# Kernel tuning notes

Measured on AMD Instinct MI355X. Metric: run time of the kernel, lower is better.

Reference implementation:

```python
import jax, jax.numpy as jnp
import numpy as np
from jax import lax

B, N, T, H, V, C = 256, 196, 26, 512, 12000, 1000


def setup_inputs() -> dict:
    key = jax.random.key(0)
    ks = jax.random.split(key, 24)
    g = lambda i, shape, s=0.02: jax.random.normal(ks[i], shape, jnp.float32) * s
    z = lambda *shape: jnp.zeros(shape, jnp.float32)
    return {
        "image": jax.random.normal(ks[0], (B, N, H), jnp.float32),
        "question": jax.random.randint(ks[1], (B, T), 0, V, jnp.int32),
        "embed_table": g(2, (V, H), 1.0),
        "W_img": g(3, (H, H)), "b_img": z(H),
        "W_uni": g(4, (1, H, H)), "b_uni": z(H),
        "W_bi": g(5, (2, H, H)), "b_bi": z(H),
        "W_tri": g(6, (3, H, H)), "b_tri": z(H),
        "lstm_k": g(7, (H, 4 * H)), "lstm_rk": g(8, (H, 4 * H)), "lstm_b": z(4 * H),
        "W_corr": g(9, (H, H)), "b_corr": z(H),
        "W_qe": g(10, (H, H)), "b_qe": z(H),
        "W_ie": g(11, (H, H)), "b_ie": z(H),
        "w_qa": g(12, (H, 1)), "b_qa": z(1),
        "w_ia": g(13, (H, 1)), "b_ia": z(1),
        "W_w": g(14, (H, H)), "b_w": z(H),
        "W_p": g(15, (2 * H, H)), "b_p": z(H),
        "W_s": g(16, (2 * H, H)), "b_s": z(H),
        "W_fc1": g(17, (H, 2 * H)), "b_fc1": z(2 * H),
        "W_fc": g(18, (2 * H, C)), "b_fc": z(C),
    }


def _conv1d(x, w, b, dil):
    # x: [B,T,H], w: [k, in, out] (WIO). TF 'same' padding == XLA SAME.
    y = lax.conv_general_dilated(x, w, window_strides=(1,), padding='SAME',
                                 rhs_dilation=(dil,),
                                 dimension_numbers=('NWC', 'WIO', 'NWC'))
    return y + b


def _lstm(x, k, rk, b):
    # Keras LSTM, gate order i,f,c,o; inference (dropout off).
    xp = jnp.einsum('bth,hg->btg', x, k) + b  # [B,T,4H]
    h0 = jnp.zeros((x.shape[0], rk.shape[0]), x.dtype)

    def step(carry, xt):
        h, c = carry
        zg = xt + h @ rk
        i, f, g, o = jnp.split(zg, 4, axis=-1)
        i, f, o = jax.nn.sigmoid(i), jax.nn.sigmoid(f), jax.nn.sigmoid(o)
        c = f * c + i * jnp.tanh(g)
        h = o * jnp.tanh(c)
        return (h, c), h

    _, hs = lax.scan(step, (h0, h0), jnp.swapaxes(xp, 0, 1))
    return jnp.swapaxes(hs, 0, 1)  # [B,T,H]


def _co_attention(img_feat, ques_feat, W_corr, b_corr, W_qe, b_qe, W_ie, b_ie,
                  w_qa, b_qa, w_ia, b_ia):
    img_corr = img_feat @ W_corr + b_corr                       # [B,N,H]
    wm = jnp.tanh(jnp.einsum('btd,bnd->btn', ques_feat, img_corr))  # affinity
    ques_embed = ques_feat @ W_qe + b_qe                        # [B,T,H]
    img_embed = img_feat @ W_ie + b_ie                          # [B,N,H]
    ques_sum = jnp.tanh(jnp.einsum('btn,bnd->btd', wm, img_embed) + ques_embed)
    ques_att = jax.nn.softmax((ques_sum @ w_qa + b_qa)[..., 0], axis=-1)  # [B,T]
    img_sum = jnp.tanh(jnp.einsum('btn,btd->bnd', wm, ques_embed) + img_embed)
    img_att = jax.nn.softmax((img_sum @ w_ia + b_ia)[..., 0], axis=-1)    # [B,N]
    q_feat = jnp.einsum('bt,btd->bd', ques_att, ques_feat)
    v_feat = jnp.einsum('bn,bnd->bd', img_att, img_feat)
    return v_feat, q_feat


def reference(image, question, embed_table, W_img, b_img, W_uni, b_uni, W_bi, b_bi,
              W_tri, b_tri, lstm_k, lstm_rk, lstm_b, W_corr, b_corr, W_qe, b_qe,
              W_ie, b_ie, w_qa, b_qa, w_ia, b_ia, W_w, b_w, W_p, b_p, W_s, b_s,
              W_fc1, b_fc1, W_fc, b_fc):
    img = jnp.tanh(image @ W_img + b_img)                       # [B,N,H]
    words = embed_table[question]                               # [B,T,H]
    uni = jnp.tanh(_conv1d(words, W_uni, b_uni, 1))
    bi = jnp.tanh(_conv1d(words, W_bi, b_bi, 2))
    tri = jnp.tanh(_conv1d(words, W_tri, b_tri, 2))
    phrase = jnp.tanh(jnp.maximum(jnp.maximum(uni, bi), tri))   # maxpool over 3 n-grams
    sentence = _lstm(phrase, lstm_k, lstm_rk, lstm_b)
    ca = lambda v, q: _co_attention(v, q, W_corr, b_corr, W_qe, b_qe, W_ie, b_ie,
                                    w_qa, b_qa, w_ia, b_ia)
    v_word, q_word = ca(img, words)
    v_phr, q_phr = ca(img, phrase)
    v_sent, q_sent = ca(img, sentence)
    h_w = jnp.tanh((q_word + v_word) @ W_w + b_w)
    h_p = jnp.tanh(jnp.concatenate([q_phr + v_phr, h_w], axis=1) @ W_p + b_p)
    h_s = jnp.tanh(jnp.concatenate([q_sent + v_sent, h_p], axis=1) @ W_s + b_s)
    fc1 = jax.nn.relu(h_s @ W_fc1 + b_fc1)
    return jax.nn.softmax(fc1 @ W_fc + b_fc, axis=-1)           # [B,C]
```

## Files before the change

### kernel.cpp

```cpp
#include <hip/hip_runtime.h>
#include <hip/hip_bf16.h>
#include <math.h>

#define Bq   256
#define Nimg 196
#define Tseq 26
#define Hd   512
#define H4   2048
#define Ccls 1000
#define KP   1536

typedef int   int4v  __attribute__((ext_vector_type(4)));
typedef float f32x4  __attribute__((ext_vector_type(4)));

#define SWZ8(x) ((x) ^ (((x) >> 3) & 7))

__device__ __forceinline__ float fast_tanh(float x) {
    float e = __expf(2.0f * x);
    return 1.0f - 2.0f * __builtin_amdgcn_rcpf(e + 1.0f);
}
__device__ __forceinline__ float fast_sigmoid(float x) {
    return __builtin_amdgcn_rcpf(1.0f + __expf(-x));
}

__device__ __forceinline__ short f2bf(float x) {
    union { float f; unsigned u; } a; a.f = x;
    unsigned r = a.u + 0x7FFF + ((a.u >> 16) & 1);
    return (short)(r >> 16);
}
__device__ __forceinline__ float bf2f(short b) {
    union { float f; unsigned u; } a; a.u = ((unsigned)(unsigned short)b) << 16;
    return a.f;
}

__global__ void embed_kernel(const int* __restrict__ q, const float* __restrict__ table,
                             short* __restrict__ words2) {
    int row = blockIdx.x;
    int tok = q[row];
    int c4 = threadIdx.x * 4;
    float4 v = *reinterpret_cast<const float4*>(table + (size_t)tok * Hd + c4);
    short h0 = f2bf(v.x), h1 = f2bf(v.y), h2 = f2bf(v.z), h3 = f2bf(v.w);
    short l0 = f2bf(v.x - bf2f(h0)), l1 = f2bf(v.y - bf2f(h1));
    short l2 = f2bf(v.z - bf2f(h2)), l3 = f2bf(v.w - bf2f(h3));
    *reinterpret_cast<short4*>(words2 + (size_t)row * 1024 + c4) = make_short4(h0, h1, h2, h3);
    *reinterpret_cast<short4*>(words2 + (size_t)row * 1024 + 512 + c4) = make_short4(l0, l1, l2, l3);
}

__global__ void split_kernel(const float* __restrict__ X, short* __restrict__ X2) {
    int i4 = blockIdx.x * 256 + threadIdx.x;
    int m = i4 >> 7, c4 = (i4 & 127) * 4;
    float4 v = *reinterpret_cast<const float4*>(X + ((size_t)m << 9) + c4);
    short h0 = f2bf(v.x), h1 = f2bf(v.y), h2 = f2bf(v.z), h3 = f2bf(v.w);
    short l0 = f2bf(v.x - bf2f(h0)), l1 = f2bf(v.y - bf2f(h1));
    short l2 = f2bf(v.z - bf2f(h2)), l3 = f2bf(v.w - bf2f(h3));
    *reinterpret_cast<short4*>(X2 + (size_t)m * 1024 + c4) = make_short4(h0, h1, h2, h3);
    *reinterpret_cast<short4*>(X2 + (size_t)m * 1024 + 512 + c4) = make_short4(l0, l1, l2, l3);
}

__global__ __launch_bounds__(256) void wsplit_all_kernel(
    const float* __restrict__ W_img, const float* __restrict__ W_corr,
    const float* __restrict__ W_ie, const float* __restrict__ W_qe,
    const float* __restrict__ W_uni, const float* __restrict__ W_bi,
    const float* __restrict__ W_tri, const float* __restrict__ lstm_k,
    short* __restrict__ WimgT2, short* __restrict__ WcorrT2,
    short* __restrict__ WieT2, short* __restrict__ WqeT2,
    short* __restrict__ WconvT2, short* __restrict__ lkT2) {
    const int z = blockIdx.z;
    const float* W; short* WT2; int Nw, n0;
    const size_t HK = (size_t)Hd * KP;
    if (z < 10) {
        Nw = Hd; n0 = blockIdx.x * 64;
        switch (z) {
            case 0: W = W_img;  WT2 = WimgT2;  break;
            case 1: W = W_corr; WT2 = WcorrT2; break;
            case 2: W = W_ie;   WT2 = WieT2;   break;
            case 3: W = W_qe;   WT2 = WqeT2;   break;
            case 4: W = W_uni;                     WT2 = WconvT2 + 0 * HK; break;
            case 5: W = W_bi;                      WT2 = WconvT2 + 1 * HK; break;
            case 6: W = W_bi + (size_t)Hd * Hd;    WT2 = WconvT2 + 2 * HK; break;
            case 7: W = W_tri;                     WT2 = WconvT2 + 3 * HK; break;
            case 8: W = W_tri + (size_t)Hd * Hd;   WT2 = WconvT2 + 4 * HK; break;
            default:W = W_tri + 2 * (size_t)Hd * Hd; WT2 = WconvT2 + 5 * HK; break;
        }
    } else {
        Nw = H4; W = lstm_k; WT2 = lkT2;
        n0 = ((z - 10) * 8 + blockIdx.x) * 64;
    }
    __shared__ float tile[64][65];
    const int k0 = blockIdx.y * 64;
    const int tid = threadIdx.x;
    #pragma unroll
    for (int p = 0; p < 16; ++p) {
        int r = p * 4 + (tid >> 6);
        int c = tid & 63;
        tile[r][c] = W[(size_t)(k0 + r) * Nw + n0 + c];
    }
    __syncthreads();
    const int n = tid >> 2;
    const int ksub = (tid & 3) * 16;
    size_t base = (size_t)(n0 + n) * KP + k0 + ksub;
    #pragma unroll
    for (int k = 0; k < 16; ++k) {
        float x = tile[ksub + k][n];
        short h = f2bf(x);
        short l = f2bf(x - bf2f(h));
        WT2[base + k] = h;
        WT2[base + 512 + k] = h;
        WT2[base + 1024 + k] = l;
    }
}

__device__ __forceinline__ void mfma16(f32x4& acc, int4v a, int4v b) {
    asm volatile("v_mfma_f32_16x16x32_bf16 %0, %1, %2, %0" : "+v"(acc) : "v"(a), "v"(b));
}

template <int ACT, int OUT, int SWZ>
__global__ __launch_bounds__(256) void mfma_gemm_kernel(
    const short* __restrict__ A2, const short* __restrict__ W2T,
    const float* __restrict__ bias, float* __restrict__ C, short* __restrict__ C2,
    int M, int N) {
    __shared__ __align__(16) short Asl[2][4096];
    __shared__ __align__(16) short Bsl[2][4096];
    const int tid = threadIdx.x;
    const int lane = tid & 63, wid = tid >> 6;
    int row0, col0;
    if (SWZ) {
        const int P8 = (M >> 7) >> 3;
        const int Cn = N >> 7;
        int L = blockIdx.x;
        int xcd = L & 7, slot = L >> 3;
        row0 = (xcd * P8 + slot / Cn) << 7;
        col0 = (slot % Cn) << 7;
    } else {
        row0 = blockIdx.y * 128;
        col0 = blockIdx.x * 128;
    }
    const int wm = wid >> 1, wn = wid & 1;
    const short* ab[2]; const short* bb[2]; int koff[2];
    #pragma unroll
    for (int c = 0; c < 2; ++c) {
        int d = c * 256 + tid;
        int s = SWZ8(d);
        int fr = s >> 6, r = (s >> 2) & 15, kb = s & 3;
        koff[c] = kb * 8;
        ab[c] = A2 + (size_t)(row0 + fr * 16 + r) * 1024;
        bb[c] = W2T + (size_t)(col0 + fr * 16 + r) * KP;
    }
    auto STAGE = [&](int buf, int k0) {
        #pragma unroll
        for (int c = 0; c < 2; ++c) {
            int kk = k0 + koff[c];
            int ka = kk >= 1024 ? kk - 1024 : kk;
            __builtin_amdgcn_global_load_lds(
                (const __attribute__((address_space(1))) void*)(ab[c] + ka),
                (__attribute__((address_space(3))) void*)(&Asl[buf][(c * 256 + wid * 64) * 8]),
                16, 0, 0);
            __builtin_amdgcn_global_load_lds(
                (const __attribute__((address_space(1))) void*)(bb[c] + kk),
                (__attribute__((address_space(3))) void*)(&Bsl[buf][(c * 256 + wid * 64) * 8]),
                16, 0, 0);
        }
    };
    f32x4 acc[4][4] = {};
    STAGE(0, 0);
    int cur = 0;
    for (int k0 = 0; k0 < KP; k0 += 32) {
        if (k0 + 32 < KP) {
            STAGE(cur ^ 1, k0 + 32);
            asm volatile("s_waitcnt vmcnt(4)" ::: "memory");
        } else {
            asm volatile("s_waitcnt vmcnt(0)" ::: "memory");
        }
        __builtin_amdgcn_s_barrier();
        __builtin_amdgcn_sched_barrier(0);
        int4v af[4], bfr[4];
        #pragma unroll
        for (int f = 0; f < 4; ++f) {
            int sa = (wm * 4 + f) * 64 + (lane & 15) * 4 + (lane >> 4);
            af[f] = *reinterpret_cast<const int4v*>(&Asl[cur][SWZ8(sa) * 8]);
            int sb = (wn * 4 + f) * 64 + (lane & 15) * 4 + (lane >> 4);
            bfr[f] = *reinterpret_cast<const int4v*>(&Bsl[cur][SWZ8(sb) * 8]);
        }
        #pragma unroll
        for (int i = 0; i < 4; ++i)
            #pragma unroll
            for (int j = 0; j < 4; ++j)
                mfma16(acc[i][j], af[i], bfr[j]);
        asm volatile("s_waitcnt lgkmcnt(0)" ::: "memory");
        __builtin_amdgcn_s_barrier();
        __builtin_amdgcn_sched_barrier(0);
        cur ^= 1;
    }
    asm volatile("s_nop 7\n\ts_nop 7" ::: "memory");
    #pragma unroll
    for (int i = 0; i < 4; ++i) {
        #pragma unroll
        for (int j = 0; j < 4; ++j) {
            int colj = col0 + wn * 64 + j * 16 + (lane & 15);
            float bv = bias ? bias[colj] : 0.f;
            #pragma unroll
            for (int r = 0; r < 4; ++r) {
                int row = row0 + wm * 64 + i * 16 + (lane >> 4) * 4 + r;
                float v = acc[i][j][r] + bv;
                if (ACT == 1) v = fast_tanh(v);
                if (OUT == 0) {
                    C[(size_t)row * N + colj] = v;
                } else {
                    short h = f2bf(v), l = f2bf(v - bf2f(h));
                    C2[(size_t)row * 1024 + colj] = h;
                    C2[(size_t)row * 1024 + 512 + colj] = l;
                }
            }
        }
    }
}

__global__ __launch_bounds__(256) void wm3_mfma_kernel(
    const short* __restrict__ Q0, const short* __restrict__ Q1, const short* __restrict__ Q2,
    const short* __restrict__ icS2, float* __restrict__ wm0, float* __restrict__ wm1,
    float* __restrict__ wm2) {
    __shared__ __align__(16) short Asl[2][4096];
    __shared__ __align__(16) short Bsl[2][4096];
    const int tid = threadIdx.x;
    const int lane = tid & 63, wid = tid >> 6;
    const int col0 = blockIdx.x * 128;
    const int b = blockIdx.y;
    const int wmq = wid >> 1, wn = wid & 1;
    const short* Qsrc[3] = {Q0, Q1, Q2};
    const short* ab[2]; const short* bb[2]; int koff[2];
    #pragma unroll
    for (int c = 0; c < 2; ++c) {
        int d = c * 256 + tid;
        int s = SWZ8(d);
        int fr = s >> 6, r = (s >> 2) & 15, kb = s & 3;
        koff[c] = kb * 8;
        int arow = fr * 16 + r;
        int lvl = arow / 26, at = arow - lvl * 26;
        if (arow >= 78) { lvl = 0; at = 0; }
        ab[c] = Qsrc[lvl] + ((size_t)(b * 26 + at)) * 1024;
        int brow = col0 + fr * 16 + r;
        if (brow > 195) brow = 195;
        bb[c] = icS2 + ((size_t)(b * 196 + brow)) * 1024;
    }
    auto STAGE = [&](int buf, int k0) {
        #pragma unroll
        for (int c = 0; c < 2; ++c) {
            int kk = k0 + koff[c];
            int ka = kk >= 1024 ? kk - 1024 : kk;
            int kbv = kk >= 512 ? kk - 512 : kk;
            __builtin_amdgcn_global_load_lds(
                (const __attribute__((address_space(1))) void*)(ab[c] + ka),
                (__attribute__((address_space(3))) void*)(&Asl[buf][(c * 256 + wid * 64) * 8]),
                16, 0, 0);
            __builtin_amdgcn_global_load_lds(
                (const __attribute__((address_space(1))) void*)(bb[c] + kbv),
                (__attribute__((address_space(3))) void*)(&Bsl[buf][(c * 256 + wid * 64) * 8]),
                16, 0, 0);
        }
    };
    f32x4 acc[4][4] = {};
    STAGE(0, 0);
    int cur = 0;
    for (int k0 = 0; k0 < KP; k0 += 32) {
        if (k0 + 32 < KP) {
            STAGE(cur ^ 1, k0 + 32);
            asm volatile("s_waitcnt vmcnt(4)" ::: "memory");
        } else {
            asm volatile("s_waitcnt vmcnt(0)" ::: "memory");
        }
        __builtin_amdgcn_s_barrier();
        __builtin_amdgcn_sched_barrier(0);
        int4v af[4], bfr[4];
        #pragma unroll
        for (int f = 0; f < 4; ++f) {
            int sa = (wmq * 4 + f) * 64 + (lane & 15) * 4 + (lane >> 4);
            af[f] = *reinterpret_cast<const int4v*>(&Asl[cur][SWZ8(sa) * 8]);
            int sb = (wn * 4 + f) * 64 + (lane & 15) * 4 + (lane >> 4);
            bfr[f] = *reinterpret_cast<const int4v*>(&Bsl[cur][SWZ8(sb) * 8]);
        }
        #pragma unroll
        for (int i = 0; i < 4; ++i)
            #pragma unroll
            for (int j = 0; j < 4; ++j)
                mfma16(acc[i][j], af[i], bfr[j]);
        asm volatile("s_waitcnt lgkmcnt(0)" ::: "memory");
        __builtin_amdgcn_s_barrier();
        __builtin_amdgcn_sched_barrier(0);
        cur ^= 1;
    }
    asm volatile("s_nop 7\n\ts_nop 7" ::: "memory");
    #pragma unroll
    for (int i = 0; i < 4; ++i) {
        #pragma unroll
        for (int j = 0; j < 4; ++j) {
            int col = col0 + wn * 64 + j * 16 + (lane & 15);
            if (col >= Nimg) continue;
            #pragma unroll
            for (int r = 0; r < 4; ++r) {
                int row = wmq * 64 + i * 16 + (lane >> 4) * 4 + r;
                if (row >= 78) continue;
                int lvl = row / 26, t = row - lvl * 26;
                float* dst = (lvl == 0) ? wm0 : (lvl == 1) ? wm1 : wm2;
                dst[((size_t)(b * 26 + t)) * Nimg + col] = fast_tanh(acc[i][j][r]);
            }
        }
    }
}

__global__ void conv_combine_kernel(const float* __restrict__ Y,
                                    const float* __restrict__ bu, const float* __restrict__ bb,
                                    const float* __restrict__ bt,
                                    short* __restrict__ phrase2) {
    int idx = blockIdx.x * 256 + threadIdx.x;
    int m = idx >> 9, c = idx & 511;
    int t = m % Tseq;
    const float* Ym = Y + (size_t)m * 3072;
    float u = Ym[c] + bu[c];
    float bv = bb[c];
    if (t > 0)  bv += Ym[-3072 + 512 + c];
    if (t < 25) bv += Ym[3072 + 1024 + c];
    float tv = Ym[2048 + c] + bt[c];
    if (t > 1)  tv += Ym[-6144 + 1536 + c];
    if (t < 24) tv += Ym[6144 + 2560 + c];
    float ph = fast_tanh(fmaxf(fmaxf(fast_tanh(u), fast_tanh(bv)), fast_tanh(tv)));
    short h = f2bf(ph), l = f2bf(ph - bf2f(h));
    phrase2[(size_t)m * 1024 + c] = h;
    phrase2[(size_t)m * 1024 + 512 + c] = l;
}

template <int ACT>
__global__ __launch_bounds__(256) void gemm_kernel(
    const float* __restrict__ A, int lda,
    const float* __restrict__ W, int ldw,
    const float* __restrict__ bias,
    float* __restrict__ C, int ldc,
    int M, int Ncols, int K) {
    __shared__ float As[16][68];
    __shared__ float Ws[16][68];
    const int tid = threadIdx.x;
    const int tx4 = (tid & 15) * 4, ty4 = (tid >> 4) * 4;
    const int row0 = blockIdx.y * 64, col0 = blockIdx.x * 64;
    const int am = tid >> 2, ak = (tid & 3) * 4;
    const int wk = tid >> 4, wc = (tid & 15) * 4;
    float acc[4][4] = {};
    for (int k0 = 0; k0 < K; k0 += 16) {
        {
            int gr = row0 + am;
            float4 v = make_float4(0.f, 0.f, 0.f, 0.f);
            if (gr < M) v = *reinterpret_cast<const float4*>(A + (size_t)gr * lda + k0 + ak);
            As[ak + 0][am] = v.x; As[ak + 1][am] = v.y; As[ak + 2][am] = v.z; As[ak + 3][am] = v.w;
        }
        {
            int gc = col0 + wc;
            const float* wp = W + (size_t)(k0 + wk) * ldw + gc;
            float4 v = make_float4(0.f, 0.f, 0.f, 0.f);
            if (gc + 3 < Ncols) v = *reinterpret_cast<const float4*>(wp);
            else {
                if (gc + 0 < Ncols) v.x = wp[0];
                if (gc + 1 < Ncols) v.y = wp[1];
                if (gc + 2 < Ncols) v.z = wp[2];
                if (gc + 3 < Ncols) v.w = wp[3];
            }
            Ws[wk][wc + 0] = v.x; Ws[wk][wc + 1] = v.y; Ws[wk][wc + 2] = v.z; Ws[wk][wc + 3] = v.w;
        }
        __syncthreads();
        #pragma unroll 4
        for (int kk = 0; kk < 16; ++kk) {
            float4 a4 = *reinterpret_cast<const float4*>(&As[kk][ty4]);
            float4 b4 = *reinterpret_cast<const float4*>(&Ws[kk][tx4]);
            float a[4] = {a4.x, a4.y, a4.z, a4.w};
            float b[4] = {b4.x, b4.y, b4.z, b4.w};
            #pragma unroll
            for (int i = 0; i < 4; ++i)
                #pragma unroll
                for (int j = 0; j < 4; ++j) acc[i][j] += a[i] * b[j];
        }
        __syncthreads();
    }
    #pragma unroll
    for (int i = 0; i < 4; ++i) {
        int r = row0 + ty4 + i;
        if (r >= M) continue;
        #pragma unroll
        for (int j = 0; j < 4; ++j) {
            int c = col0 + tx4 + j;
            if (c >= Ncols) continue;
            float v = acc[i][j];
            if (bias) v += bias[c];
            if (ACT == 1) v = fast_tanh(v);
            else if (ACT == 2) v = fmaxf(v, 0.f);
            C[(size_t)r * ldc + c] = v;
        }
    }
}

__global__ __launch_bounds__(256) void lstm_gemm_kernel(
    const float* __restrict__ h, const float* __restrict__ rk, float* __restrict__ zgp) {
    __shared__ float As[16][68];
    __shared__ float Ws[16][68];
    const int tid = threadIdx.x;
    const int tx4 = (tid & 15) * 4, ty4 = (tid >> 4) * 4;
    const int col0 = blockIdx.x * 64, row0 = blockIdx.y * 64, kb = blockIdx.z * 256;
    const int am = tid >> 2, ak = (tid & 3) * 4;
    const int wk = tid >> 4, wc = (tid & 15) * 4;
    float acc[4][4] = {};
    for (int k0 = kb; k0 < kb + 256; k0 += 16) {
        {
            float4 v = *reinterpret_cast<const float4*>(h + (size_t)(row0 + am) * Hd + k0 + ak);
            As[ak + 0][am] = v.x; As[ak + 1][am] = v.y; As[ak + 2][am] = v.z; As[ak + 3][am] = v.w;
        }
        {
            *reinterpret_cast<float4*>(&Ws[wk][wc]) =
                *reinterpret_cast<const float4*>(rk + (size_t)(k0 + wk) * H4 + col0 + wc);
        }
        __syncthreads();
        #pragma unroll 4
        for (int kk = 0; kk < 16; ++kk) {
            float4 a4 = *reinterpret_cast<const float4*>(&As[kk][ty4]);
            float4 b4 = *reinterpret_cast<const float4*>(&Ws[kk][tx4]);
            float a[4] = {a4.x, a4.y, a4.z, a4.w};
            float b[4] = {b4.x, b4.y, b4.z, b4.w};
            #pragma unroll
            for (int i = 0; i < 4; ++i)
                #pragma unroll
                for (int j = 0; j < 4; ++j) acc[i][j] += a[i] * b[j];
        }
        __syncthreads();
    }
    float* dst = zgp + (size_t)blockIdx.z * (Bq * H4);
    #pragma unroll
    for (int i = 0; i < 4; ++i) {
        int r = row0 + ty4 + i;
        *reinterpret_cast<float4*>(dst + (size_t)r * H4 + col0 + tx4) =
            make_float4(acc[i][0], acc[i][1], acc[i][2], acc[i][3]);
    }
}

__global__ __launch_bounds__(256) void lstm_gates_kernel(
    const float* __restrict__ zgp, const float* __restrict__ xp,
    float* __restrict__ c, float* __restrict__ h, short* __restrict__ sent2, int t) {
    int i = blockIdx.x * 256 + threadIdx.x;
    int b = i >> 9, hh = i & 511;
    const float* xr = xp + ((size_t)b * Tseq + t) * H4;
    float z[4];
    #pragma unroll
    for (int g = 0; g < 4; ++g) {
        float s = xr[g * 512 + hh];
        #pragma unroll
        for (int kc = 0; kc < 2; ++kc)
            s += zgp[(size_t)kc * (Bq * H4) + (size_t)b * H4 + g * 512 + hh];
        z[g] = s;
    }
    float ig = fast_sigmoid(z[0]);
    float fg = fast_sigmoid(z[1]);
    float gg = fast_tanh(z[2]);
    float og = fast_sigmoid(z[3]);
    float cv = fg * c[i] + ig * gg;
    c[i] = cv;
    float hv = og * fast_tanh(cv);
    h[i] = hv;
    short hb = f2bf(hv), lb = f2bf(hv - bf2f(hb));
    sent2[((size_t)b * Tseq + t) * 1024 + hh] = hb;
    sent2[((size_t)b * Tseq + t) * 1024 + 512 + hh] = lb;
}

__global__ __launch_bounds__(256) void qlog3_kernel(
    const float* __restrict__ wm0, const float* __restrict__ wm1, const float* __restrict__ wm2,
    const float* __restrict__ Ie, const float* __restrict__ qe0, const float* __restrict__ qe1,
    const float* __restrict__ qe2, const float* __restrict__ wqa, float* __restrict__ qlogp) {
    const int b = blockIdx.x, chunk = blockIdx.y;
    __shared__ float wms[3][Tseq][Nimg];
    __shared__ float red[4][40];
    const int tid = threadIdx.x;
    const float* wsrc[3] = {wm0, wm1, wm2};
    for (int e = tid; e < 3 * 1274; e += 256) {
        int c = e / 1274, r = e % 1274;
        *reinterpret_cast<float4*>(&wms[c][0][0] + 4 * r) =
            *reinterpret_cast<const float4*>(wsrc[c] + (size_t)b * (Tseq * Nimg) + 4 * r);
    }
    __syncthreads();
    const int hl = tid & 127, thalf = tid >> 7, tt0 = thalf * 13;
    const int h1 = chunk * 256 + hl, h2 = h1 + 128;
    float acc[3][13][2] = {};
    const float* iep1 = Ie + (size_t)b * Nimg * Hd + h1;
    const float* iep2 = Ie + (size_t)b * Nimg * Hd + h2;
    for (int n4 = 0; n4 < 49; ++n4) {
        float ieA0 = iep1[(size_t)(4 * n4 + 0) * Hd];
        float ieA1 = iep1[(size_t)(4 * n4 + 1) * Hd];
        float ieA2 = iep1[(size_t)(4 * n4 + 2) * Hd];
        float ieA3 = iep1[(size_t)(4 * n4 + 3) * Hd];
        float ieB0 = iep2[(size_t)(4 * n4 + 0) * Hd];
        float ieB1 = iep2[(size_t)(4 * n4 + 1) * Hd];
        float ieB2 = iep2[(size_t)(4 * n4 + 2) * Hd];
        float ieB3 = iep2[(size_t)(4 * n4 + 3) * Hd];
        #pragma unroll
        for (int c = 0; c < 3; ++c)
            #pragma unroll
            for (int tt = 0; tt < 13; ++tt) {
                float4 w4 = *reinterpret_cast<const float4*>(&wms[c][tt0 + tt][4 * n4]);
                acc[c][tt][0] += w4.x * ieA0 + w4.y * ieA1 + w4.z * ieA2 + w4.w * ieA3;
                acc[c][tt][1] += w4.x * ieB0 + w4.y * ieB1 + w4.z * ieB2 + w4.w * ieB3;
            }
    }
    const float wq1 = wqa[h1], wq2 = wqa[h2];
    const int lane = tid & 63, w = tid >> 6;
    const float* qes[3] = {qe0, qe1, qe2};
    #pragma unroll
    for (int c = 0; c < 3; ++c)
        #pragma unroll
        for (int tt = 0; tt < 13; ++tt) {
            int t = tt0 + tt;
            const float* qrow = qes[c] + ((size_t)(b * 26 + t)) * Hd;
            float v = fast_tanh(acc[c][tt][0] + qrow[h1]) * wq1 +
                      fast_tanh(acc[c][tt][1] + qrow[h2]) * wq2;
            #pragma unroll
            for (int off = 32; off; off >>= 1) v += __shfl_xor(v, off);
            if (lane == 0) red[w][c * 13 + tt] = v;
        }
    __syncthreads();
    if (tid < 39) {
        int c = tid / 13, tt = tid % 13;
        qlogp[((size_t)c * Bq + b) * (2 * 26) + chunk * 26 + tt] = red[0][tid] + red[1][tid];
    } else if (tid >= 64 && tid < 103) {
        int id = tid - 64;
        int c = id / 13, tt = id % 13;
        qlogp[((size_t)c * Bq + b) * (2 * 26) + chunk * 26 + 13 + tt] = red[2][id] + red[3][id];
    }
}

__global__ __launch_bounds__(256) void ilog3_kernel(
    const float* __restrict__ wmb, const float* __restrict__ qeb,
    const float* __restrict__ Ie, const float* __restrict__ wia,
    float* __restrict__ ilog3) {
    const int b = blockIdx.x, nbase = blockIdx.y * 98, lvl = blockIdx.z;
    const float* wm = wmb + (size_t)lvl * Bq * Tseq * Nimg;
    const float* qe = qeb + (size_t)lvl * Bq * Tseq * Hd;
    float* ilog = ilog3 + (size_t)lvl * Bq * Nimg;
    __shared__ float qes[Tseq][516];
    __shared__ __align__(16) float wms[Tseq][104];
    const int tid = threadIdx.x;
    for (int e = tid; e < Tseq * 128; e += 256) {
        int t = e >> 7, q4 = (e & 127) * 4;
        *reinterpret_cast<float4*>(&qes[t][q4]) =
            *reinterpret_cast<const float4*>(qe + ((size_t)(b * 26 + t)) * Hd + q4);
    }
    for (int e = tid; e < Tseq * 100; e += 256) {
        int t = e / 100, n = e % 100;
        wms[t][n] = (n < 98 && nbase + n < Nimg)
                    ? wm[((size_t)(b * 26 + t)) * Nimg + nbase + n] : 0.f;
    }
    __syncthreads();
    const int lane = tid & 63, w = tid >> 6;
    float4 wi0 = *reinterpret_cast<const float4*>(wia + 4 * lane);
    float4 wi1 = *reinterpret_cast<const float4*>(wia + 256 + 4 * lane);
    for (int n0 = w * 4; n0 < 98; n0 += 16) {
        float4 a0[4], a1[4];
        #pragma unroll
        for (int i = 0; i < 4; ++i) {
            a0[i] = make_float4(0.f, 0.f, 0.f, 0.f);
            a1[i] = make_float4(0.f, 0.f, 0.f, 0.f);
        }
        #pragma unroll 2
        for (int t = 0; t < Tseq; ++t) {
            float4 wv = *reinterpret_cast<const float4*>(&wms[t][n0]);
            float4 q0 = *reinterpret_cast<const float4*>(&qes[t][4 * lane]);
            float4 q1 = *reinterpret_cast<const float4*>(&qes[t][256 + 4 * lane]);
            float wvv[4] = {wv.x, wv.y, wv.z, wv.w};
            #pragma unroll
            for (int i = 0; i < 4; ++i) {
                a0[i].x += wvv[i] * q0.x; a0[i].y += wvv[i] * q0.y;
                a0[i].z += wvv[i] * q0.z; a0[i].w += wvv[i] * q0.w;
                a1[i].x += wvv[i] * q1.x; a1[i].y += wvv[i] * q1.y;
                a1[i].z += wvv[i] * q1.z; a1[i].w += wvv[i] * q1.w;
            }
        }
        #pragma unroll
        for (int i = 0; i < 4; ++i) {
            int n = n0 + i;
            if (n >= 98 || nbase + n >= Nimg) continue;
            const float* iebn = Ie + ((size_t)(b * Nimg) + nbase + n) * Hd;
            float4 e0 = *reinterpret_cast<const float4*>(iebn + 4 * lane);
            float4 e1 = *reinterpret_cast<const float4*>(iebn + 256 + 4 * lane);
            float v = fast_tanh(a0[i].x + e0.x) * wi0.x + fast_tanh(a0[i].y + e0.y) * wi0.y +
                      fast_tanh(a0[i].z + e0.z) * wi0.z + fast_tanh(a0[i].w + e0.w) * wi0.w +
                      fast_tanh(a1[i].x + e1.x) * wi1.x + fast_tanh(a1[i].y + e1.y) * wi1.y +
                      fast_tanh(a1[i].z + e1.z) * wi1.z + fast_tanh(a1[i].w + e1.w) * wi1.w;
            #pragma unroll
            for (int off = 32; off; off >>= 1) v += __shfl_xor(v, off);
            if (lane == 0) ilog[(size_t)b * Nimg + nbase + n] = v;
        }
    }
}

__global__ void softmaxT_part_kernel(const float* __restrict__ lgp, float* __restrict__ att) {
    int b = blockIdx.x, c = blockIdx.y, lane = threadIdx.x;
    float v = -INFINITY;
    if (lane < Tseq) {
        const float* p = lgp + ((size_t)c * Bq + b) * (2 * 26) + lane;
        v = p[0] + p[26];
    }
    float m = v;
    #pragma unroll
    for (int off = 32; off; off >>= 1) m = fmaxf(m, __shfl_xor(m, off));
    float e = (lane < Tseq) ? __expf(v - m) : 0.f;
    float s = e;
    #pragma unroll
    for (int off = 32; off; off >>= 1) s += __shfl_xor(s, off);
    if (lane < Tseq) att[((size_t)c * Bq + b) * Tseq + lane] = e / s;
}

__global__ void softmax_N_kernel(const float* __restrict__ lg, float* __restrict__ att) {
    int b = blockIdx.x, c = blockIdx.y, lane = threadIdx.x;
    const float* lb = lg + ((size_t)c * Bq + b) * Nimg;
    float* ab = att + ((size_t)c * Bq + b) * Nimg;
    float v[4]; float m = -INFINITY;
    #pragma unroll
    for (int k = 0; k < 4; ++k) {
        int n = lane + 64 * k;
        v[k] = (n < Nimg) ? lb[n] : -INFINITY;
        m = fmaxf(m, v[k]);
    }
    #pragma unroll
    for (int off = 32; off; off >>= 1) m = fmaxf(m, __shfl_xor(m, off));
    float e[4]; float s = 0.f;
    #pragma unroll
    for (int k = 0; k < 4; ++k) {
        int n = lane + 64 * k;
        e[k] = (n < Nimg) ? __expf(v[k] - m) : 0.f;
        s += e[k];
    }
    #pragma unroll
    for (int off = 32; off; off >>= 1) s += __shfl_xor(s, off);
    #pragma unroll
    for (int k = 0; k < 4; ++k) {
        int n = lane + 64 * k;
        if (n < Nimg) ab[n] = e[k] / s;
    }
}

__global__ __launch_bounds__(256) void feat3_kernel(
    const float* __restrict__ qatt0, const float* __restrict__ qatt1, const float* __restrict__ qatt2,
    const float* __restrict__ iatt0, const float* __restrict__ iatt1, const float* __restrict__ iatt2,
    const short* __restrict__ Qw2, const short* __restrict__ Qp2, const short* __restrict__ Qs2,
    const short* __restrict__ img2, float* __restrict__ s_part) {
    const int b = blockIdx.x, chunk = blockIdx.y, tid = threadIdx.x;
    float a[3][2] = {};
    if (chunk == 0) {
        for (int t = 0; t < Tseq; ++t) {
            float w0 = qatt0[b * Tseq + t], w1 = qatt1[b * Tseq + t], w2 = qatt2[b * Tseq + t];
            const short* p0 = Qw2 + ((size_t)(b * Tseq + t)) * 1024;
            const short* p1 = Qp2 + ((size_t)(b * Tseq + t)) * 1024;
            const short* p2 = Qs2 + ((size_t)(b * Tseq + t)) * 1024;
            a[0][0] += w0 * (bf2f(p0[tid]) + bf2f(p0[512 + tid]));
            a[0][1] += w0 * (bf2f(p0[256 + tid]) + bf2f(p0[768 + tid]));
            a[1][0] += w1 * (bf2f(p1[tid]) + bf2f(p1[512 + tid]));
            a[1][1] += w1 * (bf2f(p1[256 + tid]) + bf2f(p1[768 + tid]));
            a[2][0] += w2 * (bf2f(p2[tid]) + bf2f(p2[512 + tid]));
            a[2][1] += w2 * (bf2f(p2[256 + tid]) + bf2f(p2[768 + tid]));
        }
    }
    int ns, ne;
    if (chunk == 0)      { ns = 0;   ne = 30;  }
    else if (chunk == 1) { ns = 30;  ne = 86;  }
    else if (chunk == 2) { ns = 86;  ne = 141; }
    else                 { ns = 141; ne = 196; }
    for (int n = ns; n < ne; ++n) {
        float w0 = iatt0[b * Nimg + n], w1 = iatt1[b * Nimg + n], w2 = iatt2[b * Nimg + n];
        const short* p = img2 + ((size_t)(b * Nimg) + n) * 1024;
        float v0 = bf2f(p[tid]) + bf2f(p[512 + tid]);
        float v1 = bf2f(p[256 + tid]) + bf2f(p[768 + tid]);
        a[0][0] += w0 * v0; a[0][1] += w0 * v1;
        a[1][0] += w1 * v0; a[1][1] += w1 * v1;
        a[2][0] += w2 * v0; a[2][1] += w2 * v1;
    }
    #pragma unroll
    for (int c = 0; c < 3; ++c) {
        float* dst = s_part + ((size_t)(chunk * 3 + c) * Bq + b) * Hd;
        dst[tid] = a[c][0];
        dst[tid + 256] = a[c][1];
    }
}

__global__ void feat_combine_kernel(const float* __restrict__ s_part, float* __restrict__ s0,
                                    float* __restrict__ s1, float* __restrict__ s2) {
    int i = blockIdx.x * 256 + threadIdx.x;
    int c = i / (Bq * Hd), r = i % (Bq * Hd);
    float v = 0.f;
    #pragma unroll
    for (int ch = 0; ch < 4; ++ch) v += s_part[(size_t)(ch * 3 + c) * (Bq * Hd) + r];
    float* dst = (c == 0) ? s0 : (c == 1) ? s1 : s2;
    dst[r] = v;
}

__global__ void concat_kernel(const float* __restrict__ x, const float* __restrict__ y,
                              float* __restrict__ out) {
    int i = blockIdx.x * 256 + threadIdx.x;
    int b = i >> 9, j = i & 511;
    out[(size_t)b * 1024 + j] = x[i];
    out[(size_t)b * 1024 + 512 + j] = y[i];
}

__global__ __launch_bounds__(256) void softmax_C_kernel(const float* __restrict__ lg,
                                                        float* __restrict__ out) {
    int b = blockIdx.x, tid = threadIdx.x;
    __shared__ float red[4];
    const float* lb = lg + (size_t)b * Ccls;
    float v[4]; float m = -INFINITY;
    #pragma unroll
    for (int k = 0; k < 4; ++k) {
        int j = tid + 256 * k;
        v[k] = (j < Ccls) ? lb[j] : -INFINITY;
        m = fmaxf(m, v[k]);
    }
    #pragma unroll
    for (int off = 32; off; off >>= 1) m = fmaxf(m, __shfl_xor(m, off));
    int lane = tid & 63, w = tid >> 6;
    if (lane == 0) red[w] = m;
    __syncthreads();
    m = fmaxf(fmaxf(red[0], red[1]), fmaxf(red[2], red[3]));
    __syncthreads();
    float e[4]; float s = 0.f;
    #pragma unroll
    for (int k = 0; k < 4; ++k) {
        int j = tid + 256 * k;
        e[k] = (j < Ccls) ? __expf(v[k] - m) : 0.f;
        s += e[k];
    }
    #pragma unroll
    for (int off = 32; off; off >>= 1) s += __shfl_xor(s, off);
    if (lane == 0) red[w] = s;
    __syncthreads();
    s = red[0] + red[1] + red[2] + red[3];
    float inv = 1.f / s;
    #pragma unroll
    for (int k = 0; k < 4; ++k) {
        int j = tid + 256 * k;
        if (j < Ccls) out[(size_t)b * Ccls + j] = e[k] * inv;
    }
}

extern "C" void kernel_launch(void* const* d_in, const int* in_sizes, int n_in,
                              void* d_out, int out_size, void* d_ws, size_t ws_size,
                              hipStream_t stream) {
    const float* image   = (const float*)d_in[0];
    const int*   question= (const int*)  d_in[1];
    const float* embed   = (const float*)d_in[2];
    const float* W_img   = (const float*)d_in[3];
    const float* b_img   = (const float*)d_in[4];
    const float* W_uni   = (const float*)d_in[5];
    const float* b_uni   = (const float*)d_in[6];
    const float* W_bi    = (const float*)d_in[7];
    const float* b_bi    = (const float*)d_in[8];
    const float* W_tri   = (const float*)d_in[9];
    const float* b_tri   = (const float*)d_in[10];
    const float* lstm_k  = (const float*)d_in[11];
    const float* lstm_rk = (const float*)d_in[12];
    const float* lstm_b  = (const float*)d_in[13];
    const float* W_corr  = (const float*)d_in[14];
    const float* b_corr  = (const float*)d_in[15];
    const float* W_qe    = (const float*)d_in[16];
    const float* b_qe    = (const float*)d_in[17];
    const float* W_ie    = (const float*)d_in[18];
    const float* b_ie    = (const float*)d_in[19];
    const float* w_qa    = (const float*)d_in[20];
    const float* w_ia    = (const float*)d_in[22];
    const float* W_w     = (const float*)d_in[24];
    const float* b_w     = (const float*)d_in[25];
    const float* W_p     = (const float*)d_in[26];
    const float* b_p     = (const float*)d_in[27];
    const float* W_s     = (const float*)d_in[28];
    const float* b_s     = (const float*)d_in[29];
    const float* W_fc1   = (const float*)d_in[30];
    const float* b_fc1   = (const float*)d_in[31];
    const float* W_fc    = (const float*)d_in[32];
    const float* b_fc    = (const float*)d_in[33];

    float* p = (float*)d_ws;
    size_t off = 0;
    auto take = [&](size_t n) { float* r = p + off; off += n; return r; };
    auto take_s = [&](size_t n) { short* r = (short*)(p + off); off += n / 2; return r; };
    float* bufB   = take((size_t)Bq * Nimg * Hd);
    float* xp     = take((size_t)Bq * Tseq * H4);
    float* wm0    = take((size_t)Bq * Tseq * Nimg);
    float* wm1    = take((size_t)Bq * Tseq * Nimg);
    float* wm2    = take((size_t)Bq * Tseq * Nimg);
    float* hbuf   = take((size_t)Bq * Hd);
    float* cbuf   = take((size_t)Bq * Hd);
    float* zgp    = take((size_t)2 * Bq * H4);
    float* qlogp  = take((size_t)3 * Bq * 4 * Tseq);
    float* qatt0  = take((size_t)Bq * Tseq);
    float* qatt1  = take((size_t)Bq * Tseq);
    float* qatt2  = take((size_t)Bq * Tseq);
    float* ilog3  = take((size_t)3 * Bq * Nimg);
    float* iatt0  = take((size_t)Bq * Nimg);
    float* iatt1  = take((size_t)Bq * Nimg);
    float* iatt2  = take((size_t)Bq * Nimg);
    short* imgS2   = take_s((size_t)Bq * Nimg * 1024);
    short* words2  = take_s((size_t)Bq * Tseq * 1024);
    short* phrase2 = take_s((size_t)Bq * Tseq * 1024);
    short* sentn2  = take_s((size_t)Bq * Tseq * 1024);
    short* WimgT2  = take_s((size_t)Hd * KP);
    short* WcorrT2 = take_s((size_t)Hd * KP);
    short* WieT2   = take_s((size_t)Hd * KP);
    short* WqeT2   = take_s((size_t)Hd * KP);
    short* WconvT2 = take_s((size_t)6 * Hd * KP);
    short* lkT2    = take_s((size_t)H4 * KP);

    float* qe0 = xp;
    float* qe1 = xp + (size_t)Bq * Tseq * Hd;
    float* qe2 = xp + 2 * (size_t)Bq * Tseq * Hd;
    float* s_part = xp + 3 * (size_t)Bq * Tseq * Hd;
    float* Y      = bufB;
    short* image2 = (short*)bufB;
    short* icS2   = (short*)bufB;
    float* catb   = wm0;
    float* fc1b   = wm0 + (size_t)Bq * 2 * Hd;
    float* logits = wm0 + 2 * (size_t)Bq * 2 * Hd;
    float* s0     = wm1;
    float* s1     = wm1 + 1 * (size_t)Bq * Hd;
    float* s2     = wm1 + 2 * (size_t)Bq * Hd;
    float* hw     = wm1 + 3 * (size_t)Bq * Hd;
    float* hp     = wm1 + 4 * (size_t)Bq * Hd;
    float* hsv    = wm1 + 5 * (size_t)Bq * Hd;

    const int MI = Bq * Nimg;
    const int MT = Bq * Tseq;

    wsplit_all_kernel<<<dim3(8, 8, 14), 256, 0, stream>>>(
        W_img, W_corr, W_ie, W_qe, W_uni, W_bi, W_tri, lstm_k,
        WimgT2, WcorrT2, WieT2, WqeT2, WconvT2, lkT2);

    embed_kernel<<<MT, 128, 0, stream>>>(question, embed, words2);
    split_kernel<<<MI / 2, 256, 0, stream>>>(image, image2);
    mfma_gemm_kernel<1, 1, 1><<<dim3((MI / 128) * (Hd / 128)), 256, 0, stream>>>(
        image2, WimgT2, b_img, nullptr, imgS2, MI, Hd);
    mfma_gemm_kernel<0, 0, 0><<<dim3(3072 / 128, MT / 128), 256, 0, stream>>>(
        words2, WconvT2, nullptr, Y, nullptr, MT, 3072);
    conv_combine_kernel<<<(MT * Hd) / 256, 256, 0, stream>>>(Y, b_uni, b_bi, b_tri, phrase2);
    mfma_gemm_kernel<0, 0, 0><<<dim3(H4 / 128, MT / 128), 256, 0, stream>>>(
        phrase2, lkT2, lstm_b, xp, nullptr, MT, H4);
    hipMemsetAsync(hbuf, 0, (size_t)Bq * Hd * sizeof(float), stream);
    hipMemsetAsync(cbuf, 0, (size_t)Bq * Hd * sizeof(float), stream);
    for (int t = 0; t < Tseq; ++t) {
        lstm_gemm_kernel<<<dim3(32, 4, 2), 256, 0, stream>>>(hbuf, lstm_rk, zgp);
        lstm_gates_kernel<<<(Bq * Hd) / 256, 256, 0, stream>>>(zgp, xp, cbuf, hbuf, sentn2, t);
    }
    mfma_gemm_kernel<0, 1, 1><<<dim3((MI / 128) * (Hd / 128)), 256, 0, stream>>>(
        imgS2, WcorrT2, b_corr, nullptr, icS2, MI, Hd);
    wm3_mfma_kernel<<<dim3(2, Bq), 256, 0, stream>>>(words2, phrase2, sentn2, icS2,
                                                     wm0, wm1, wm2);
    mfma_gemm_kernel<0, 0, 1><<<dim3((MI / 128) * (Hd / 128)), 256, 0, stream>>>(
        imgS2, WieT2, b_ie, bufB, nullptr, MI, Hd);
    mfma_gemm_kernel<0, 0, 0><<<dim3(Hd / 128, (3 * MT) / 128), 256, 0, stream>>>(
        words2, WqeT2, b_qe, qe0, nullptr, 3 * MT, Hd);
    qlog3_kernel<<<dim3(Bq, 2), 256, 0, stream>>>(wm0, wm1, wm2, bufB, qe0, qe1, qe2, w_qa, qlogp);
    softmaxT_part_kernel<<<dim3(Bq, 3), 64, 0, stream>>>(qlogp, qatt0);
    ilog3_kernel<<<dim3(Bq, 2, 3), 256, 0, stream>>>(wm0, qe0, bufB, w_ia, ilog3);
    softmax_N_kernel<<<dim3(Bq, 3), 64, 0, stream>>>(ilog3, iatt0);
    feat3_kernel<<<dim3(Bq, 4), 256, 0, stream>>>(qatt0, qatt1, qatt2, iatt0, iatt1, iatt2,
                                                  words2, phrase2, sentn2, imgS2, s_part);
    feat_combine_kernel<<<(3 * Bq * Hd) / 256, 256, 0, stream>>>(s_part, s0, s1, s2);
    gemm_kernel<1><<<dim3(Hd / 64, Bq / 64), 256, 0, stream>>>(
        s0, Hd, W_w, Hd, b_w, hw, Hd, Bq, Hd, Hd);
    concat_kernel<<<(Bq * Hd) / 256, 256, 0, stream>>>(s1, hw, catb);
    gemm_kernel<1><<<dim3(Hd / 64, Bq / 64), 256, 0, stream>>>(
        catb, 2 * Hd, W_p, Hd, b_p, hp, Hd, Bq, Hd, 2 * Hd);
    concat_kernel<<<(Bq * Hd) / 256, 256, 0, stream>>>(s2, hp, catb);
    gemm_kernel<1><<<dim3(Hd / 64, Bq / 64), 256, 0, stream>>>(
        catb, 2 * Hd, W_s, Hd, b_s, hsv, Hd, Bq, Hd, 2 * Hd);
    gemm_kernel<2><<<dim3((2 * Hd) / 64, Bq / 64), 256, 0, stream>>>(
        hsv, Hd, W_fc1, 2 * Hd, b_fc1, fc1b, 2 * Hd, Bq, 2 * Hd, Hd);
    gemm_kernel<0><<<dim3((Ccls + 63) / 64, Bq / 64), 256, 0, stream>>>(
        fc1b, 2 * Hd, W_fc, Ccls, b_fc, logits, Ccls, Bq, Ccls, 2 * Hd);
    softmax_C_kernel<<<Bq, 256, 0, stream>>>(logits, (float*)d_out);
}
```

Before: 1.883 ms.

## Apply W_corr to question features instead of image, split ilog over hidden halves

Reassociates the correlation product so W_corr multiplies the 3x26 question rows (about 20K rows) instead of all 196 image rows per batch (about 50K rows). The bias is folded in through a per-row dot product with b_corr added before tanh in the affinity kernel. The ilog kernel is also split across two halves of the hidden dimension to double its grid, and the two partial sums are added inside the softmax. This saves a large GEMM but adds a small qb kernel and an extra partial-logit buffer.

```diff
diff --git a/kernel.cpp b/kernel.cpp
--- a/kernel.cpp
+++ b/kernel.cpp
@@ -9,6 +9,7 @@
 #define H4   2048
 #define Ccls 1000
 #define KP   1536
+#define MT3  19968
 
 typedef int   int4v  __attribute__((ext_vector_type(4)));
 typedef float f32x4  __attribute__((ext_vector_type(4)));
@@ -62,17 +63,34 @@
     const float* __restrict__ W_ie, const float* __restrict__ W_qe,
     const float* __restrict__ W_uni, const float* __restrict__ W_bi,
     const float* __restrict__ W_tri, const float* __restrict__ lstm_k,
-    short* __restrict__ WimgT2, short* __restrict__ WcorrT2,
+    short* __restrict__ WimgT2, short* __restrict__ WcorrR2,
     short* __restrict__ WieT2, short* __restrict__ WqeT2,
     short* __restrict__ WconvT2, short* __restrict__ lkT2) {
     const int z = blockIdx.z;
+    const int tid = threadIdx.x;
+    const int k0 = blockIdx.y * 64;
+    const size_t HK = (size_t)Hd * KP;
+    if (z == 1) {
+        const int n0 = blockIdx.x * 64;
+        const int n = tid >> 2, ksub = (tid & 3) * 16;
+        const float* src = W_corr + (size_t)(n0 + n) * Hd + k0 + ksub;
+        size_t base = (size_t)(n0 + n) * KP + k0 + ksub;
+        #pragma unroll
+        for (int k = 0; k < 16; ++k) {
+            float x = src[k];
+            short h = f2bf(x);
+            short l = f2bf(x - bf2f(h));
+            WcorrR2[base + k] = h;
+            WcorrR2[base + 512 + k] = h;
+            WcorrR2[base + 1024 + k] = l;
+        }
+        return;
+    }
     const float* W; short* WT2; int Nw, n0;
-    const size_t HK = (size_t)Hd * KP;
     if (z < 10) {
         Nw = Hd; n0 = blockIdx.x * 64;
         switch (z) {
             case 0: W = W_img;  WT2 = WimgT2;  break;
-            case 1: W = W_corr; WT2 = WcorrT2; break;
             case 2: W = W_ie;   WT2 = WieT2;   break;
             case 3: W = W_qe;   WT2 = WqeT2;   break;
             case 4: W = W_uni;                     WT2 = WconvT2 + 0 * HK; break;
@@ -87,8 +105,6 @@
         n0 = ((z - 10) * 8 + blockIdx.x) * 64;
     }
     __shared__ float tile[64][65];
-    const int k0 = blockIdx.y * 64;
-    const int tid = threadIdx.x;
     #pragma unroll
     for (int p = 0; p < 16; ++p) {
         int r = p * 4 + (tid >> 6);
@@ -108,6 +124,23 @@
         WT2[base + 512 + k] = h;
         WT2[base + 1024 + k] = l;
     }
+}
+
+__global__ __launch_bounds__(256) void qb_kernel(const short* __restrict__ Q2,
+                                                 const float* __restrict__ b_corr,
+                                                 float* __restrict__ qb) {
+    const int tid = threadIdx.x, lane = tid & 63, wid = tid >> 6;
+    const int r = blockIdx.x * 4 + wid;
+    const short* row = Q2 + (size_t)r * 1024 + lane * 8;
+    float v = 0.f;
+    #pragma unroll
+    for (int k = 0; k < 8; ++k) {
+        float x = bf2f(row[k]) + bf2f(row[512 + k]);
+        v += x * b_corr[lane * 8 + k];
+    }
+    #pragma unroll
+    for (int off = 32; off; off >>= 1) v += __shfl_xor(v, off);
+    if (lane == 0) qb[r] = v;
 }
 
 __device__ __forceinline__ void mfma16(f32x4& acc, int4v a, int4v b) {
@@ -216,8 +249,8 @@
 }
 
 __global__ __launch_bounds__(256) void wm3_mfma_kernel(
-    const short* __restrict__ Q0, const short* __restrict__ Q1, const short* __restrict__ Q2,
-    const short* __restrict__ icS2, float* __restrict__ wm0, float* __restrict__ wm1,
+    const short* __restrict__ Qc2, const short* __restrict__ img2,
+    const float* __restrict__ qb, float* __restrict__ wm0, float* __restrict__ wm1,
     float* __restrict__ wm2) {
     __shared__ __align__(16) short Asl[2][4096];
     __shared__ __align__(16) short Bsl[2][4096];
@@ -226,7 +259,6 @@
     const int col0 = blockIdx.x * 128;
     const int b = blockIdx.y;
     const int wmq = wid >> 1, wn = wid & 1;
-    const short* Qsrc[3] = {Q0, Q1, Q2};
     const short* ab[2]; const short* bb[2]; int koff[2];
     #pragma unroll
     for (int c = 0; c < 2; ++c) {
@@ -237,10 +269,10 @@
         int arow = fr * 16 + r;
         int lvl = arow / 26, at = arow - lvl * 26;
         if (arow >= 78) { lvl = 0; at = 0; }
-        ab[c] = Qsrc[lvl] + ((size_t)(b * 26 + at)) * 1024;
+        ab[c] = Qc2 + ((size_t)lvl * (Bq * Tseq) + (size_t)(b * 26 + at)) * 1024;
         int brow = col0 + fr * 16 + r;
         if (brow > 195) brow = 195;
-        bb[c] = icS2 + ((size_t)(b * 196 + brow)) * 1024;
+        bb[c] = img2 + ((size_t)(b * 196 + brow)) * 1024;
     }
     auto STAGE = [&](int buf, int k0) {
         #pragma unroll
@@ -301,7 +333,8 @@
                 if (row >= 78) continue;
                 int lvl = row / 26, t = row - lvl * 26;
                 float* dst = (lvl == 0) ? wm0 : (lvl == 1) ? wm1 : wm2;
-                dst[((size_t)(b * 26 + t)) * Nimg + col] = fast_tanh(acc[i][j][r]);
+                float qbv = qb[(size_t)lvl * (Bq * Tseq) + b * 26 + t];
+                dst[((size_t)(b * 26 + t)) * Nimg + col] = fast_tanh(acc[i][j][r] + qbv);
             }
         }
     }
@@ -531,18 +564,20 @@
 __global__ __launch_bounds__(256) void ilog3_kernel(
     const float* __restrict__ wmb, const float* __restrict__ qeb,
     const float* __restrict__ Ie, const float* __restrict__ wia,
-    float* __restrict__ ilog3) {
-    const int b = blockIdx.x, nbase = blockIdx.y * 98, lvl = blockIdx.z;
+    float* __restrict__ ilogp) {
+    const int b = blockIdx.x, lvl = blockIdx.z;
+    const int nbase = (blockIdx.y & 1) * 98, hc = blockIdx.y >> 1;
+    const int hbase = hc * 256;
     const float* wm = wmb + (size_t)lvl * Bq * Tseq * Nimg;
     const float* qe = qeb + (size_t)lvl * Bq * Tseq * Hd;
-    float* ilog = ilog3 + (size_t)lvl * Bq * Nimg;
-    __shared__ float qes[Tseq][516];
+    float* ilog = ilogp + (size_t)hc * (3 * Bq * Nimg) + (size_t)lvl * Bq * Nimg;
+    __shared__ float qes[Tseq][260];
     __shared__ __align__(16) float wms[Tseq][104];
     const int tid = threadIdx.x;
-    for (int e = tid; e < Tseq * 128; e += 256) {
-        int t = e >> 7, q4 = (e & 127) * 4;
+    for (int e = tid; e < Tseq * 64; e += 256) {
+        int t = e >> 6, q4 = (e & 63) * 4;
         *reinterpret_cast<float4*>(&qes[t][q4]) =
-            *reinterpret_cast<const float4*>(qe + ((size_t)(b * 26 + t)) * Hd + q4);
+            *reinterpret_cast<const float4*>(qe + ((size_t)(b * 26 + t)) * Hd + hbase + q4);
     }
     for (int e = tid; e < Tseq * 100; e += 256) {
         int t = e / 100, n = e % 100;
@@ -551,40 +586,30 @@
     }
     __syncthreads();
     const int lane = tid & 63, w = tid >> 6;
-    float4 wi0 = *reinterpret_cast<const float4*>(wia + 4 * lane);
-    float4 wi1 = *reinterpret_cast<const float4*>(wia + 256 + 4 * lane);
+    float4 wi = *reinterpret_cast<const float4*>(wia + hbase + 4 * lane);
     for (int n0 = w * 4; n0 < 98; n0 += 16) {
-        float4 a0[4], a1[4];
-        #pragma unroll
-        for (int i = 0; i < 4; ++i) {
-            a0[i] = make_float4(0.f, 0.f, 0.f, 0.f);
-            a1[i] = make_float4(0.f, 0.f, 0.f, 0.f);
-        }
+        float4 a0[4];
+        #pragma unroll
+        for (int i = 0; i < 4; ++i) a0[i] = make_float4(0.f, 0.f, 0.f, 0.f);
         #pragma unroll 2
         for (int t = 0; t < Tseq; ++t) {
             float4 wv = *reinterpret_cast<const float4*>(&wms[t][n0]);
             float4 q0 = *reinterpret_cast<const float4*>(&qes[t][4 * lane]);
-            float4 q1 = *reinterpret_cast<const float4*>(&qes[t][256 + 4 * lane]);
             float wvv[4] = {wv.x, wv.y, wv.z, wv.w};
             #pragma unroll
             for (int i = 0; i < 4; ++i) {
                 a0[i].x += wvv[i] * q0.x; a0[i].y += wvv[i] * q0.y;
                 a0[i].z += wvv[i] * q0.z; a0[i].w += wvv[i] * q0.w;
-                a1[i].x += wvv[i] * q1.x; a1[i].y += wvv[i] * q1.y;
-                a1[i].z += wvv[i] * q1.z; a1[i].w += wvv[i] * q1.w;
             }
         }
         #pragma unroll
         for (int i = 0; i < 4; ++i) {
             int n = n0 + i;
             if (n >= 98 || nbase + n >= Nimg) continue;
-            const float* iebn = Ie + ((size_t)(b * Nimg) + nbase + n) * Hd;
+            const float* iebn = Ie + ((size_t)(b * Nimg) + nbase + n) * Hd + hbase;
             float4 e0 = *reinterpret_cast<const float4*>(iebn + 4 * lane);
-            float4 e1 = *reinterpret_cast<const float4*>(iebn + 256 + 4 * lane);
-            float v = fast_tanh(a0[i].x + e0.x) * wi0.x + fast_tanh(a0[i].y + e0.y) * wi0.y +
-                      fast_tanh(a0[i].z + e0.z) * wi0.z + fast_tanh(a0[i].w + e0.w) * wi0.w +
-                      fast_tanh(a1[i].x + e1.x) * wi1.x + fast_tanh(a1[i].y + e1.y) * wi1.y +
-                      fast_tanh(a1[i].z + e1.z) * wi1.z + fast_tanh(a1[i].w + e1.w) * wi1.w;
+            float v = fast_tanh(a0[i].x + e0.x) * wi.x + fast_tanh(a0[i].y + e0.y) * wi.y +
+                      fast_tanh(a0[i].z + e0.z) * wi.z + fast_tanh(a0[i].w + e0.w) * wi.w;
             #pragma unroll
             for (int off = 32; off; off >>= 1) v += __shfl_xor(v, off);
             if (lane == 0) ilog[(size_t)b * Nimg + nbase + n] = v;
@@ -611,13 +636,14 @@
 
 __global__ void softmax_N_kernel(const float* __restrict__ lg, float* __restrict__ att) {
     int b = blockIdx.x, c = blockIdx.y, lane = threadIdx.x;
-    const float* lb = lg + ((size_t)c * Bq + b) * Nimg;
+    const float* lb0 = lg + ((size_t)c * Bq + b) * Nimg;
+    const float* lb1 = lb0 + (size_t)3 * Bq * Nimg;
     float* ab = att + ((size_t)c * Bq + b) * Nimg;
     float v[4]; float m = -INFINITY;
     #pragma unroll
     for (int k = 0; k < 4; ++k) {
         int n = lane + 64 * k;
-        v[k] = (n < Nimg) ? lb[n] : -INFINITY;
+        v[k] = (n < Nimg) ? (lb0[n] + lb1[n]) : -INFINITY;
         m = fmaxf(m, v[k]);
     }
     #pragma unroll
@@ -791,16 +817,17 @@
     float* qatt0  = take((size_t)Bq * Tseq);
     float* qatt1  = take((size_t)Bq * Tseq);
     float* qatt2  = take((size_t)Bq * Tseq);
-    float* ilog3  = take((size_t)3 * Bq * Nimg);
+    float* ilogp  = take((size_t)2 * 3 * Bq * Nimg);
     float* iatt0  = take((size_t)Bq * Nimg);
     float* iatt1  = take((size_t)Bq * Nimg);
     float* iatt2  = take((size_t)Bq * Nimg);
+    float* qb     = take((size_t)MT3);
     short* imgS2   = take_s((size_t)Bq * Nimg * 1024);
     short* words2  = take_s((size_t)Bq * Tseq * 1024);
     short* phrase2 = take_s((size_t)Bq * Tseq * 1024);
     short* sentn2  = take_s((size_t)Bq * Tseq * 1024);
     short* WimgT2  = take_s((size_t)Hd * KP);
-    short* WcorrT2 = take_s((size_t)Hd * KP);
+    short* WcorrR2 = take_s((size_t)Hd * KP);
     short* WieT2   = take_s((size_t)Hd * KP);
     short* WqeT2   = take_s((size_t)Hd * KP);
     short* WconvT2 = take_s((size_t)6 * Hd * KP);
@@ -812,7 +839,7 @@
     float* s_part = xp + 3 * (size_t)Bq * Tseq * Hd;
     float* Y      = bufB;
     short* image2 = (short*)bufB;
-    short* icS2   = (short*)bufB;
+    short* Qc2    = (short*)bufB;
     float* catb   = wm0;
     float* fc1b   = wm0 + (size_t)Bq * 2 * Hd;
     float* logits = wm0 + 2 * (size_t)Bq * 2 * Hd;
@@ -828,7 +855,7 @@
 
     wsplit_all_kernel<<<dim3(8, 8, 14), 256, 0, stream>>>(
         W_img, W_corr, W_ie, W_qe, W_uni, W_bi, W_tri, lstm_k,
-        WimgT2, WcorrT2, WieT2, WqeT2, WconvT2, lkT2);
+        WimgT2, WcorrR2, WieT2, WqeT2, WconvT2, lkT2);
 
     embed_kernel<<<MT, 128, 0, stream>>>(question, embed, words2);
     split_kernel<<<MI / 2, 256, 0, stream>>>(image, image2);
@@ -845,18 +872,18 @@
         lstm_gemm_kernel<<<dim3(32, 4, 2), 256, 0, stream>>>(hbuf, lstm_rk, zgp);
         lstm_gates_kernel<<<(Bq * Hd) / 256, 256, 0, stream>>>(zgp, xp, cbuf, hbuf, sentn2, t);
     }
-    mfma_gemm_kernel<0, 1, 1><<<dim3((MI / 128) * (Hd / 128)), 256, 0, stream>>>(
-        imgS2, WcorrT2, b_corr, nullptr, icS2, MI, Hd);
-    wm3_mfma_kernel<<<dim3(2, Bq), 256, 0, stream>>>(words2, phrase2, sentn2, icS2,
-                                                     wm0, wm1, wm2);
+    qb_kernel<<<MT3 / 4, 256, 0, stream>>>(words2, b_corr, qb);
+    mfma_gemm_kernel<0, 1, 0><<<dim3(Hd / 128, MT3 / 128), 256, 0, stream>>>(
+        words2, WcorrR2, nullptr, nullptr, Qc2, MT3, Hd);
+    wm3_mfma_kernel<<<dim3(2, Bq), 256, 0, stream>>>(Qc2, imgS2, qb, wm0, wm1, wm2);
     mfma_gemm_kernel<0, 0, 1><<<dim3((MI / 128) * (Hd / 128)), 256, 0, stream>>>(
         imgS2, WieT2, b_ie, bufB, nullptr, MI, Hd);
-    mfma_gemm_kernel<0, 0, 0><<<dim3(Hd / 128, (3 * MT) / 128), 256, 0, stream>>>(
-        words2, WqeT2, b_qe, qe0, nullptr, 3 * MT, Hd);
+    mfma_gemm_kernel<0, 0, 0><<<dim3(Hd / 128, MT3 / 128), 256, 0, stream>>>(
+        words2, WqeT2, b_qe, qe0, nullptr, MT3, Hd);
     qlog3_kernel<<<dim3(Bq, 2), 256, 0, stream>>>(wm0, wm1, wm2, bufB, qe0, qe1, qe2, w_qa, qlogp);
     softmaxT_part_kernel<<<dim3(Bq, 3), 64, 0, stream>>>(qlogp, qatt0);
-    ilog3_kernel<<<dim3(Bq, 2, 3), 256, 0, stream>>>(wm0, qe0, bufB, w_ia, ilog3);
-    softmax_N_kernel<<<dim3(Bq, 3), 64, 0, stream>>>(ilog3, iatt0);
+    ilog3_kernel<<<dim3(Bq, 4, 3), 256, 0, stream>>>(wm0, qe0, bufB, w_ia, ilogp);
+    softmax_N_kernel<<<dim3(Bq, 3), 64, 0, stream>>>(ilogp, iatt0);
     feat3_kernel<<<dim3(Bq, 4), 256, 0, stream>>>(qatt0, qatt1, qatt2, iatt0, iatt1, iatt2,
                                                   words2, phrase2, sentn2, imgS2, s_part);
     feat_combine_kernel<<<(3 * Bq * Hd) / 256, 256, 0, stream>>>(s_part, s0, s1, s2);
```

Result: faster. 1.816 ms (median of 2 runs) (-3.5%).
